# Kernel tuning notes

Hardware: AMD Instinct MI355X
Metric: run time of the kernel (lower is better)

The kernel has to match this reference:

```python
import jax, jax.numpy as jnp
import numpy as np

EPS = 1e-8  # torch cosine_similarity eps


def setup_inputs() -> dict:
    key = jax.random.key(0)
    kq, km = jax.random.split(key)
    B, N, D = 256, 100000, 1024
    query = jax.random.normal(kq, (B, D), dtype=jnp.float32)
    memory = jax.random.normal(km, (N, D), dtype=jnp.float32)
    return {"query": query, "memory": memory, "k": 16}


def reference(query, memory, k):
    # Batched, fused version of HierarchicalMemory.retrieve():
    # cosine similarity of each query against every stored module, then top-k.
    # sim(q, m) = q.m / max(||q||*||m||, eps), matching F.cosine_similarity.
    qn = jnp.linalg.norm(query, axis=-1)          # [B]
    mn = jnp.linalg.norm(memory, axis=-1)         # [N]
    dots = jnp.einsum("bd,nd->bn", query, memory)  # [B, N]
    sims = dots / jnp.maximum(qn[:, None] * mn[None, :], EPS)
    top_vals, top_idx = jax.lax.top_k(sims, k)    # [B, k] each
    return top_vals, top_idx
```

## Files before the change

kernel.cpp:

```cpp
#include <hip/hip_runtime.h>
#include <math.h>

#define DDIM 1024
#define BQ 256
#define EPSV 1e-8f
#define CH 4
#define TPC 32
#define NCAND (CH * TPC)

typedef short bf16x8 __attribute__((ext_vector_type(8)));
typedef float f32x4 __attribute__((ext_vector_type(4)));

__device__ __forceinline__ unsigned short f2bf(float x) {
  union { float f; unsigned int u; } v;
  v.f = x;
  unsigned int lsb = (v.u >> 16) & 1u;
  v.u += 0x7fffu + lsb;
  return (unsigned short)(v.u >> 16);
}
__device__ __forceinline__ float bf2f(unsigned short b) {
  union { unsigned int u; float f; } v;
  v.u = ((unsigned int)b) << 16;
  return v.f;
}
__device__ __forceinline__ unsigned int cvtpk_bf16(float lo, float hi) {
  unsigned int r;
  asm("v_cvt_pk_bf16_f32 %0, %1, %2" : "=v"(r) : "v"(lo), "v"(hi));
  return r;
}

__global__ __launch_bounds__(256) void prep_q(const float* __restrict__ Q,
                                              unsigned short* __restrict__ Qb,
                                              float* __restrict__ qn) {
  int wave = threadIdx.x >> 6, lane = threadIdx.x & 63;
  int q = blockIdx.x * 4 + wave;
  const float4* src = (const float4*)(Q + (size_t)q * DDIM);
  int g = q >> 4, qrow = q & 15;
  float s = 0.f;
#pragma unroll
  for (int t4 = 0; t4 < 4; ++t4) {
    float4 v = src[t4 * 64 + lane];
    s += v.x * v.x + v.y * v.y + v.z * v.z + v.w * v.w;
    int k = t4 * 256 + lane * 4;
    int tt = k >> 5;
    int kquad = (k >> 3) & 3;
    int elem = k & 7;
    size_t chunk = (size_t)(tt * 16 + g) * 64 + kquad * 16 + qrow;
    ushort4 o;
    o.x = f2bf(v.x); o.y = f2bf(v.y); o.z = f2bf(v.z); o.w = f2bf(v.w);
    *(ushort4*)(Qb + chunk * 8 + elem) = o;
  }
#pragma unroll
  for (int o = 32; o > 0; o >>= 1) s += __shfl_down(s, o, 64);
  if (lane == 0) qn[q] = sqrtf(s);
}

__global__ __launch_bounds__(256) void gemm_topk(
    const float* __restrict__ M, const unsigned short* __restrict__ Qb,
    unsigned short* __restrict__ sims, float* __restrict__ rmn,
    int N, int Npitch) {
  __shared__ unsigned short Ms[2][64 * 32];
  const int tid = threadIdx.x;
  const int wave = tid >> 6, lane = tid & 63;
  const int quad = lane >> 4, l15 = lane & 15;
  const int n0 = blockIdx.x * 64;

  const int mrow = tid >> 2;
  const int mchunk = tid & 3;
  const bool mvalid = (n0 + mrow) < N;
  const float* mptr = M + (size_t)(mvalid ? (n0 + mrow) : 0) * DDIM + mchunk * 8;

  const bf16x8* qptr = (const bf16x8*)Qb + (size_t)wave * 256 + lane;

  f32x4 acc[4][4];
#pragma unroll
  for (int i = 0; i < 4; ++i)
#pragma unroll
    for (int j = 0; j < 4; ++j) acc[i][j] = (f32x4){0.f, 0.f, 0.f, 0.f};
  float sumsq = 0.f;

  bf16x8 aA0 = qptr[0], aA1 = qptr[64], aA2 = qptr[128], aA3 = qptr[192];
  bf16x8 aB0{}, aB1{}, aB2{}, aB3{};
  float4 mrA0 = *(const float4*)(mptr);
  float4 mrA1 = *(const float4*)(mptr + 4);
  float4 mrB0 = *(const float4*)(mptr + 32);
  float4 mrB1 = *(const float4*)(mptr + 36);

  auto body = [&](int t, int buf, float4& r0, float4& r1, bf16x8& c0,
                  bf16x8& c1, bf16x8& c2, bf16x8& c3, bf16x8& p0, bf16x8& p1,
                  bf16x8& p2, bf16x8& p3) {
    sumsq += r0.x * r0.x + r0.y * r0.y + r0.z * r0.z + r0.w * r0.w +
             r1.x * r1.x + r1.y * r1.y + r1.z * r1.z + r1.w * r1.w;
    uint4 packed;
    packed.x = cvtpk_bf16(r0.x, r0.y);
    packed.y = cvtpk_bf16(r0.z, r0.w);
    packed.z = cvtpk_bf16(r1.x, r1.y);
    packed.w = cvtpk_bf16(r1.z, r1.w);
    *(uint4*)&Ms[buf][mrow * 32 + mchunk * 8] = packed;
    int k2 = t * 32 + 64;
    const float* p = mptr + ((k2 < DDIM) ? k2 : 0);
    r0 = *(const float4*)(p);
    r1 = *(const float4*)(p + 4);
    asm volatile("s_waitcnt lgkmcnt(0)" ::: "memory");
    __builtin_amdgcn_s_barrier();
    __builtin_amdgcn_sched_barrier(0);
    const bf16x8* qp = qptr + (size_t)((t + 1) & 31) * 1024;
    p0 = qp[0]; p1 = qp[64]; p2 = qp[128]; p3 = qp[192];
    bf16x8 bfr[4];
#pragma unroll
    for (int j = 0; j < 4; ++j)
      bfr[j] = *(const bf16x8*)&Ms[buf][(j * 16 + l15) * 32 + quad * 8];
    acc[0][0] = __builtin_amdgcn_mfma_f32_16x16x32_bf16(c0, bfr[0], acc[0][0], 0, 0, 0);
    acc[0][1] = __builtin_amdgcn_mfma_f32_16x16x32_bf16(c0, bfr[1], acc[0][1], 0, 0, 0);
    acc[0][2] = __builtin_amdgcn_mfma_f32_16x16x32_bf16(c0, bfr[2], acc[0][2], 0, 0, 0);
    acc[0][3] = __builtin_amdgcn_mfma_f32_16x16x32_bf16(c0, bfr[3], acc[0][3], 0, 0, 0);
    acc[1][0] = __builtin_amdgcn_mfma_f32_16x16x32_bf16(c1, bfr[0], acc[1][0], 0, 0, 0);
    acc[1][1] = __builtin_amdgcn_mfma_f32_16x16x32_bf16(c1, bfr[1], acc[1][1], 0, 0, 0);
    acc[1][2] = __builtin_amdgcn_mfma_f32_16x16x32_bf16(c1, bfr[2], acc[1][2], 0, 0, 0);
    acc[1][3] = __builtin_amdgcn_mfma_f32_16x16x32_bf16(c1, bfr[3], acc[1][3], 0, 0, 0);
    acc[2][0] = __builtin_amdgcn_mfma_f32_16x16x32_bf16(c2, bfr[0], acc[2][0], 0, 0, 0);
    acc[2][1] = __builtin_amdgcn_mfma_f32_16x16x32_bf16(c2, bfr[1], acc[2][1], 0, 0, 0);
    acc[2][2] = __builtin_amdgcn_mfma_f32_16x16x32_bf16(c2, bfr[2], acc[2][2], 0, 0, 0);
    acc[2][3] = __builtin_amdgcn_mfma_f32_16x16x32_bf16(c2, bfr[3], acc[2][3], 0, 0, 0);
    acc[3][0] = __builtin_amdgcn_mfma_f32_16x16x32_bf16(c3, bfr[0], acc[3][0], 0, 0, 0);
    acc[3][1] = __builtin_amdgcn_mfma_f32_16x16x32_bf16(c3, bfr[1], acc[3][1], 0, 0, 0);
    acc[3][2] = __builtin_amdgcn_mfma_f32_16x16x32_bf16(c3, bfr[2], acc[3][2], 0, 0, 0);
    acc[3][3] = __builtin_amdgcn_mfma_f32_16x16x32_bf16(c3, bfr[3], acc[3][3], 0, 0, 0);
  };

#pragma unroll 1
  for (int t = 0; t < 32; t += 2) {
    body(t, 0, mrA0, mrA1, aA0, aA1, aA2, aA3, aB0, aB1, aB2, aB3);
    body(t + 1, 1, mrB0, mrB1, aB0, aB1, aB2, aB3, aA0, aA1, aA2, aA3);
  }

  float s = sumsq;
  s += __shfl_xor(s, 1, 64);
  s += __shfl_xor(s, 2, 64);
  if (mchunk == 0) rmn[n0 + mrow] = (s > 0.f) ? rsqrtf(s) : 0.f;

#pragma unroll
  for (int i = 0; i < 4; ++i)
#pragma unroll
    for (int j = 0; j < 4; ++j)
#pragma unroll
      for (int r = 0; r < 4; ++r) {
        int q = wave * 64 + i * 16 + quad * 4 + r;
        int n = n0 + j * 16 + l15;
        sims[(size_t)q * Npitch + n] = f2bf(acc[i][j][r]);
      }
}

__device__ __forceinline__ bool better(float v1, int i1, float v2, int i2) {
  return v1 > v2 || (v1 == v2 && i1 < i2);
}

template <int L>
__device__ __forceinline__ void insert_topL(float (&tv)[L], int (&ti)[L],
                                            float v, int idx) {
  if (v > tv[L - 1] || (v == tv[L - 1] && idx < ti[L - 1])) {
    tv[L - 1] = v; ti[L - 1] = idx;
#pragma unroll
    for (int j = L - 1; j > 0; --j) {
      if (better(tv[j], ti[j], tv[j - 1], ti[j - 1])) {
        float fv = tv[j]; tv[j] = tv[j - 1]; tv[j - 1] = fv;
        int ii = ti[j]; ti[j] = ti[j - 1]; ti[j - 1] = ii;
      }
    }
  }
}

template <int L, typename F>
__device__ __forceinline__ void block_extract(float (&tv)[L], int (&ti)[L],
                                              int rounds, F&& emit) {
  __shared__ float s_v[4];
  __shared__ int s_i[4];
  __shared__ int s_t[4];
  __shared__ float s_wv;
  __shared__ int s_wi;
  __shared__ int s_wt;
  for (int r = 0; r < rounds; ++r) {
    float v = tv[0];
    int idx = ti[0];
    int src = threadIdx.x;
#pragma unroll
    for (int o = 32; o > 0; o >>= 1) {
      float ov = __shfl_down(v, o, 64);
      int oi = __shfl_down(idx, o, 64);
      int os = __shfl_down(src, o, 64);
      if (better(ov, oi, v, idx)) { v = ov; idx = oi; src = os; }
    }
    int lane = threadIdx.x & 63, w = threadIdx.x >> 6;
    if (lane == 0) { s_v[w] = v; s_i[w] = idx; s_t[w] = src; }
    __syncthreads();
    if (threadIdx.x == 0) {
      float bv = s_v[0]; int bi = s_i[0]; int bt = s_t[0];
      for (int w2 = 1; w2 < 4; ++w2)
        if (better(s_v[w2], s_i[w2], bv, bi)) { bv = s_v[w2]; bi = s_i[w2]; bt = s_t[w2]; }
      s_wv = bv; s_wi = bi; s_wt = bt;
    }
    __syncthreads();
    if (threadIdx.x == s_wt) {
#pragma unroll
      for (int j = 0; j < L - 1; ++j) { tv[j] = tv[j + 1]; ti[j] = ti[j + 1]; }
      tv[L - 1] = -INFINITY; ti[L - 1] = 0x7fffffff;
    }
    if (threadIdx.x == 0) emit(r, s_wv, s_wi);
    __syncthreads();
  }
}

__global__ __launch_bounds__(256) void select_chunks(
    const unsigned short* __restrict__ sims, const float* __restrict__ rmn,
    int* __restrict__ cand, int N, int Npitch, int Nc) {
  int q = blockIdx.y;
  int c = blockIdx.x;
  int start = c * Nc;
  int end = start + Nc;
  if (end > N) end = N;
  float tv[8]; int ti[8];
#pragma unroll
  for (int j = 0; j < 8; ++j) { tv[j] = -INFINITY; ti[j] = 0x7fffffff; }
  const unsigned short* row = sims + (size_t)q * Npitch;
  int base = start + threadIdx.x * 8;
  for (; base + 8 <= end; base += 2048) {
    uint4 wv = *(const uint4*)(row + base);
    float4 r0 = *(const float4*)&rmn[base];
    float4 r1 = *(const float4*)&rmn[base + 4];
    float f0 = bf2f((unsigned short)(wv.x & 0xffff)) * r0.x;
    float f1 = bf2f((unsigned short)(wv.x >> 16)) * r0.y;
    float f2 = bf2f((unsigned short)(wv.y & 0xffff)) * r0.z;
    float f3 = bf2f((unsigned short)(wv.y >> 16)) * r0.w;
    float f4 = bf2f((unsigned short)(wv.z & 0xffff)) * r1.x;
    float f5 = bf2f((unsigned short)(wv.z >> 16)) * r1.y;
    float f6 = bf2f((unsigned short)(wv.w & 0xffff)) * r1.z;
    float f7 = bf2f((unsigned short)(wv.w >> 16)) * r1.w;
    insert_topL<8>(tv, ti, f0, base + 0);
    insert_topL<8>(tv, ti, f1, base + 1);
    insert_topL<8>(tv, ti, f2, base + 2);
    insert_topL<8>(tv, ti, f3, base + 3);
    insert_topL<8>(tv, ti, f4, base + 4);
    insert_topL<8>(tv, ti, f5, base + 5);
    insert_topL<8>(tv, ti, f6, base + 6);
    insert_topL<8>(tv, ti, f7, base + 7);
  }
  if (base < end) {
    for (int n = base; n < end; ++n)
      insert_topL<8>(tv, ti, bf2f(row[n]) * rmn[n], n);
  }
  int* dst = cand + (size_t)q * NCAND + c * TPC;
  block_extract<8>(tv, ti, TPC, [&](int r, float v, int i) {
    dst[r] = (i == 0x7fffffff) ? 0 : i;
  });
}

__global__ __launch_bounds__(512) void rescore(
    const float* __restrict__ Q, const float* __restrict__ M,
    const float* __restrict__ qn, const int* __restrict__ cand,
    float* __restrict__ out, int N) {
  __shared__ float cosv[NCAND];
  __shared__ int cidx[NCAND];
  int q = blockIdx.x;
  int wave = threadIdx.x >> 6, lane = threadIdx.x & 63;
  const float4* qf4 = (const float4*)(Q + (size_t)q * DDIM);
  float4 qv[4];
#pragma unroll
  for (int t = 0; t < 4; ++t) qv[t] = qf4[t * 64 + lane];
  float qnv = qn[q];
#pragma unroll 1
  for (int i = 0; i < NCAND / 8; ++i) {
    int c = wave * (NCAND / 8) + i;
    int idx = cand[(size_t)q * NCAND + c];
    if (idx < 0 || idx >= N) idx = 0;
    const float4* mf4 = (const float4*)(M + (size_t)idx * DDIM);
    float dot = 0.f, sq = 0.f;
#pragma unroll
    for (int t = 0; t < 4; ++t) {
      float4 m = mf4[t * 64 + lane];
      dot += m.x * qv[t].x + m.y * qv[t].y + m.z * qv[t].z + m.w * qv[t].w;
      sq += m.x * m.x + m.y * m.y + m.z * m.z + m.w * m.w;
    }
#pragma unroll
    for (int o = 32; o > 0; o >>= 1) {
      dot += __shfl_down(dot, o, 64);
      sq += __shfl_down(sq, o, 64);
    }
    if (lane == 0) {
      cosv[c] = dot / fmaxf(qnv * sqrtf(sq), EPSV);
      cidx[c] = idx;
    }
  }
  __syncthreads();
  if (wave == 0) {
    float v0 = cosv[lane], v1 = cosv[lane + 64];
    int i0 = cidx[lane], i1 = cidx[lane + 64];
    for (int r = 0; r < 16; ++r) {
      bool fb = better(v0, i0, v1, i1);
      float bv = fb ? v0 : v1;
      int bi = fb ? i0 : i1;
      int bs = lane * 2 + (fb ? 0 : 1);
#pragma unroll
      for (int o = 32; o > 0; o >>= 1) {
        float ov = __shfl_down(bv, o, 64);
        int oi = __shfl_down(bi, o, 64);
        int os = __shfl_down(bs, o, 64);
        if (better(ov, oi, bv, bi)) { bv = ov; bi = oi; bs = os; }
      }
      bv = __shfl(bv, 0, 64);
      bi = __shfl(bi, 0, 64);
      bs = __shfl(bs, 0, 64);
      if (lane == (bs >> 1)) {
        if (bs & 1) v1 = -INFINITY; else v0 = -INFINITY;
      }
      if (lane == 0) {
        out[(size_t)q * 16 + r] = bv;
        out[(size_t)BQ * 16 + (size_t)q * 16 + r] = (float)bi;
      }
    }
  }
}

extern "C" void kernel_launch(void* const* d_in, const int* in_sizes, int n_in,
                              void* d_out, int out_size, void* d_ws, size_t ws_size,
                              hipStream_t stream) {
  const float* Q = (const float*)d_in[0];
  const float* M = (const float*)d_in[1];
  int N = in_sizes[1] / DDIM;
  float* out = (float*)d_out;

  int nb = (N + 63) / 64;
  int Npitch = nb * 64;

  char* w = (char*)d_ws;
  size_t off = 0;
  auto alloc = [&](size_t bytes) {
    char* p = w + off;
    off = (off + bytes + 255) & ~(size_t)255;
    return p;
  };
  unsigned short* Qb = (unsigned short*)alloc((size_t)BQ * DDIM * 2);
  float* qn = (float*)alloc((size_t)BQ * 4);
  float* rmn = (float*)alloc((size_t)Npitch * 4);
  int* cand = (int*)alloc((size_t)BQ * NCAND * 4);
  unsigned short* sims = (unsigned short*)alloc((size_t)BQ * Npitch * 2);
  (void)ws_size;

  int Nc = (((N + CH - 1) / CH) + 7) & ~7;

  prep_q<<<BQ / 4, 256, 0, stream>>>(Q, Qb, qn);
  gemm_topk<<<nb, 256, 0, stream>>>(M, Qb, sims, rmn, N, Npitch);
  select_chunks<<<dim3(CH, BQ), 256, 0, stream>>>(sims, rmn, cand, N, Npitch, Nc);
  rescore<<<BQ, 512, 0, stream>>>(Q, M, qn, cand, out, N);
}
```

Measured before the change: 705.3 us.

## Fuse chunked candidate selection with exact rescoring into one kernel

Merges select_chunks and rescore into a single per-query kernel with 512 threads. Each block scans the whole bf16 similarity row, extracts 48 candidates through a block-wide reduction and rescores them in fp32 from shared memory. This drops one launch and the global candidate buffer, and rescores 48 candidates instead of 128 (4 chunks of 32). The cost is fewer blocks in the selection phase (256 instead of 1024) and a smaller candidate margin against bf16 ranking errors, which could hurt accuracy.

```diff
diff --git a/kernel.cpp b/kernel.cpp
--- a/kernel.cpp
+++ b/kernel.cpp
@@ -4,9 +4,7 @@
 #define DDIM 1024
 #define BQ 256
 #define EPSV 1e-8f
-#define CH 4
-#define TPC 32
-#define NCAND (CH * TPC)
+#define NCAND 48
 
 typedef short bf16x8 __attribute__((ext_vector_type(8)));
 typedef float f32x4 __attribute__((ext_vector_type(4)));
@@ -170,60 +168,30 @@
   }
 }
 
-template <int L, typename F>
-__device__ __forceinline__ void block_extract(float (&tv)[L], int (&ti)[L],
-                                              int rounds, F&& emit) {
-  __shared__ float s_v[4];
-  __shared__ int s_i[4];
-  __shared__ int s_t[4];
+__global__ __launch_bounds__(512) void select_rescore(
+    const unsigned short* __restrict__ sims, const float* __restrict__ rmn,
+    const float* __restrict__ Q, const float* __restrict__ M,
+    const float* __restrict__ qn, float* __restrict__ out,
+    int N, int Npitch) {
+  __shared__ float s_v[8];
+  __shared__ int s_i[8];
+  __shared__ int s_t[8];
   __shared__ float s_wv;
   __shared__ int s_wi;
   __shared__ int s_wt;
-  for (int r = 0; r < rounds; ++r) {
-    float v = tv[0];
-    int idx = ti[0];
-    int src = threadIdx.x;
-#pragma unroll
-    for (int o = 32; o > 0; o >>= 1) {
-      float ov = __shfl_down(v, o, 64);
-      int oi = __shfl_down(idx, o, 64);
-      int os = __shfl_down(src, o, 64);
-      if (better(ov, oi, v, idx)) { v = ov; idx = oi; src = os; }
-    }
-    int lane = threadIdx.x & 63, w = threadIdx.x >> 6;
-    if (lane == 0) { s_v[w] = v; s_i[w] = idx; s_t[w] = src; }
-    __syncthreads();
-    if (threadIdx.x == 0) {
-      float bv = s_v[0]; int bi = s_i[0]; int bt = s_t[0];
-      for (int w2 = 1; w2 < 4; ++w2)
-        if (better(s_v[w2], s_i[w2], bv, bi)) { bv = s_v[w2]; bi = s_i[w2]; bt = s_t[w2]; }
-      s_wv = bv; s_wi = bi; s_wt = bt;
-    }
-    __syncthreads();
-    if (threadIdx.x == s_wt) {
-#pragma unroll
-      for (int j = 0; j < L - 1; ++j) { tv[j] = tv[j + 1]; ti[j] = ti[j + 1]; }
-      tv[L - 1] = -INFINITY; ti[L - 1] = 0x7fffffff;
-    }
-    if (threadIdx.x == 0) emit(r, s_wv, s_wi);
-    __syncthreads();
-  }
-}
-
-__global__ __launch_bounds__(256) void select_chunks(
-    const unsigned short* __restrict__ sims, const float* __restrict__ rmn,
-    int* __restrict__ cand, int N, int Npitch, int Nc) {
-  int q = blockIdx.y;
-  int c = blockIdx.x;
-  int start = c * Nc;
-  int end = start + Nc;
-  if (end > N) end = N;
+  __shared__ float cosv[NCAND];
+  __shared__ int cidx[NCAND];
+
+  const int q = blockIdx.x;
+  const int tid = threadIdx.x;
+  const int lane = tid & 63, wave = tid >> 6;
+
   float tv[8]; int ti[8];
 #pragma unroll
   for (int j = 0; j < 8; ++j) { tv[j] = -INFINITY; ti[j] = 0x7fffffff; }
   const unsigned short* row = sims + (size_t)q * Npitch;
-  int base = start + threadIdx.x * 8;
-  for (; base + 8 <= end; base += 2048) {
+  int base = tid * 8;
+  for (; base + 8 <= N; base += 4096) {
     uint4 wv = *(const uint4*)(row + base);
     float4 r0 = *(const float4*)&rmn[base];
     float4 r1 = *(const float4*)&rmn[base + 4];
@@ -244,33 +212,49 @@
     insert_topL<8>(tv, ti, f6, base + 6);
     insert_topL<8>(tv, ti, f7, base + 7);
   }
-  if (base < end) {
-    for (int n = base; n < end; ++n)
+  if (base < N) {
+    for (int n = base; n < N; ++n)
       insert_topL<8>(tv, ti, bf2f(row[n]) * rmn[n], n);
   }
-  int* dst = cand + (size_t)q * NCAND + c * TPC;
-  block_extract<8>(tv, ti, TPC, [&](int r, float v, int i) {
-    dst[r] = (i == 0x7fffffff) ? 0 : i;
-  });
-}
-
-__global__ __launch_bounds__(512) void rescore(
-    const float* __restrict__ Q, const float* __restrict__ M,
-    const float* __restrict__ qn, const int* __restrict__ cand,
-    float* __restrict__ out, int N) {
-  __shared__ float cosv[NCAND];
-  __shared__ int cidx[NCAND];
-  int q = blockIdx.x;
-  int wave = threadIdx.x >> 6, lane = threadIdx.x & 63;
+
+  for (int r = 0; r < NCAND; ++r) {
+    float v = tv[0];
+    int idx = ti[0];
+    int src = tid;
+#pragma unroll
+    for (int o = 32; o > 0; o >>= 1) {
+      float ov = __shfl_down(v, o, 64);
+      int oi = __shfl_down(idx, o, 64);
+      int os = __shfl_down(src, o, 64);
+      if (better(ov, oi, v, idx)) { v = ov; idx = oi; src = os; }
+    }
+    if (lane == 0) { s_v[wave] = v; s_i[wave] = idx; s_t[wave] = src; }
+    __syncthreads();
+    if (tid == 0) {
+      float bv = s_v[0]; int bi = s_i[0]; int bt = s_t[0];
+      for (int w2 = 1; w2 < 8; ++w2)
+        if (better(s_v[w2], s_i[w2], bv, bi)) { bv = s_v[w2]; bi = s_i[w2]; bt = s_t[w2]; }
+      s_wv = bv; s_wi = bi; s_wt = bt;
+      cidx[r] = (bi == 0x7fffffff) ? 0 : bi;
+    }
+    __syncthreads();
+    if (tid == s_wt) {
+#pragma unroll
+      for (int j = 0; j < 7; ++j) { tv[j] = tv[j + 1]; ti[j] = ti[j + 1]; }
+      tv[7] = -INFINITY; ti[7] = 0x7fffffff;
+    }
+    __syncthreads();
+  }
+
   const float4* qf4 = (const float4*)(Q + (size_t)q * DDIM);
   float4 qv[4];
 #pragma unroll
   for (int t = 0; t < 4; ++t) qv[t] = qf4[t * 64 + lane];
   float qnv = qn[q];
-#pragma unroll 1
+#pragma unroll 2
   for (int i = 0; i < NCAND / 8; ++i) {
     int c = wave * (NCAND / 8) + i;
-    int idx = cand[(size_t)q * NCAND + c];
+    int idx = cidx[c];
     if (idx < 0 || idx >= N) idx = 0;
     const float4* mf4 = (const float4*)(M + (size_t)idx * DDIM);
     float dot = 0.f, sq = 0.f;
@@ -287,18 +271,17 @@
     }
     if (lane == 0) {
       cosv[c] = dot / fmaxf(qnv * sqrtf(sq), EPSV);
-      cidx[c] = idx;
     }
   }
   __syncthreads();
+
   if (wave == 0) {
-    float v0 = cosv[lane], v1 = cosv[lane + 64];
-    int i0 = cidx[lane], i1 = cidx[lane + 64];
+    float v0 = (lane < NCAND) ? cosv[lane] : -INFINITY;
+    int i0 = (lane < NCAND) ? cidx[lane] : 0x7fffffff;
     for (int r = 0; r < 16; ++r) {
-      bool fb = better(v0, i0, v1, i1);
-      float bv = fb ? v0 : v1;
-      int bi = fb ? i0 : i1;
-      int bs = lane * 2 + (fb ? 0 : 1);
+      float bv = v0;
+      int bi = i0;
+      int bs = lane;
 #pragma unroll
       for (int o = 32; o > 0; o >>= 1) {
         float ov = __shfl_down(bv, o, 64);
@@ -309,9 +292,7 @@
       bv = __shfl(bv, 0, 64);
       bi = __shfl(bi, 0, 64);
       bs = __shfl(bs, 0, 64);
-      if (lane == (bs >> 1)) {
-        if (bs & 1) v1 = -INFINITY; else v0 = -INFINITY;
-      }
+      if (lane == bs) v0 = -INFINITY;
       if (lane == 0) {
         out[(size_t)q * 16 + r] = bv;
         out[(size_t)BQ * 16 + (size_t)q * 16 + r] = (float)bi;
@@ -341,14 +322,10 @@
   unsigned short* Qb = (unsigned short*)alloc((size_t)BQ * DDIM * 2);
   float* qn = (float*)alloc((size_t)BQ * 4);
   float* rmn = (float*)alloc((size_t)Npitch * 4);
-  int* cand = (int*)alloc((size_t)BQ * NCAND * 4);
   unsigned short* sims = (unsigned short*)alloc((size_t)BQ * Npitch * 2);
   (void)ws_size;
 
-  int Nc = (((N + CH - 1) / CH) + 7) & ~7;
-
   prep_q<<<BQ / 4, 256, 0, stream>>>(Q, Qb, qn);
   gemm_topk<<<nb, 256, 0, stream>>>(M, Qb, sims, rmn, N, Npitch);
-  select_chunks<<<dim3(CH, BQ), 256, 0, stream>>>(sims, rmn, cand, N, Npitch, Nc);
-  rescore<<<BQ, 512, 0, stream>>>(Q, M, qn, cand, out, N);
-}
+  select_rescore<<<BQ, 512, 0, stream>>>(sims, rmn, Q, M, qn, out, N, Npitch);
+}
```

Measured after the change: 722.0 us. 2.4% more time.
